# Performance work log

Measured on AMD Instinct MI355X. Metric: run time of the kernel, lower is better.

The kernel has to match this reference:

```python
import jax, jax.numpy as jnp
import numpy as np

N = 100000      # nodes
E = 1000000     # directed edges (before self loops)
F_IN = 64       # num_node_features
HID = 64        # hidden_channels
OUT = 32        # output_dim
NEG_SLOPE = 0.2 # PyG GATConv default


def setup_inputs() -> dict:
    key = jax.random.key(0)
    ks = jax.random.split(key, 20)
    inp = {
        "x": jax.random.normal(ks[0], (N, F_IN), jnp.float32),
        "edge_index": jax.random.randint(ks[1], (2, E), 0, N, dtype=jnp.int32),
    }
    def glorot(k, shape):
        fan = shape[0] + (shape[1] if len(shape) > 1 else 1)
        return jax.random.normal(k, shape, jnp.float32) * jnp.sqrt(2.0 / fan)
    dims = [(F_IN, HID), (HID, HID), (HID, HID)]
    i = 2
    for li, (fi, fo) in enumerate(dims, start=1):
        inp[f"W{li}"] = glorot(ks[i], (fi, fo)); i += 1
        inp[f"as{li}"] = glorot(ks[i], (fo,)); i += 1
        inp[f"ad{li}"] = glorot(ks[i], (fo,)); i += 1
        inp[f"b{li}"] = jnp.zeros((fo,), jnp.float32)
    inp["Wl"] = glorot(ks[i], (HID, OUT)); i += 1
    inp["bl"] = jnp.zeros((OUT,), jnp.float32)
    return inp


def gat_conv(h_in, W, a_src, a_dst, b, src, dst):
    """PyG GATConv, heads=1: gather -> LeakyReLU logits -> segment softmax over
    incoming edges of each destination node -> weighted scatter-add."""
    h = h_in @ W                                  # [N, C]
    alpha_s = h @ a_src                           # [N]
    alpha_d = h @ a_dst                           # [N]
    e = jax.nn.leaky_relu(alpha_s[src] + alpha_d[dst], NEG_SLOPE)  # [E']
    # numerically stable segment softmax keyed by dst
    m = jax.ops.segment_max(e, dst, num_segments=N)                # [N]
    w = jnp.exp(e - m[dst])                                        # [E']
    denom = jax.ops.segment_sum(w, dst, num_segments=N)            # [N]
    coef = w / (denom[dst] + 1e-16)                                # [E']
    out = jax.ops.segment_sum(coef[:, None] * h[src], dst, num_segments=N)
    return out + b


def reference(x, edge_index, W1, as1, ad1, b1, W2, as2, ad2, b2, W3, as3, ad3, b3, Wl, bl):
    # add_self_loops=True (PyG default): every node attends to itself too
    loops = jnp.arange(N, dtype=edge_index.dtype)
    src = jnp.concatenate([edge_index[0], loops])
    dst = jnp.concatenate([edge_index[1], loops])
    h = jax.nn.relu(gat_conv(x, W1, as1, ad1, b1, src, dst))
    # dropout(p=0.5) is identity in eval mode
    h = jax.nn.relu(gat_conv(h, W2, as2, ad2, b2, src, dst))
    h = jax.nn.relu(gat_conv(h, W3, as3, ad3, b3, src, dst))
    return h @ Wl + bl
```

## Files before the change

### kernel.cpp

```cpp
#include <hip/hip_runtime.h>
#include <hip/hip_fp16.h>
#include <math.h>

#define F 64
#define OUTF 32
#define PAD 64
#define NEG_SLOPE 0.2f
#define GBCAP 6144

typedef _Float16 half8v __attribute__((ext_vector_type(8)));
typedef float    f32x4  __attribute__((ext_vector_type(4)));

__device__ __forceinline__ float leaky(float v) {
    return (v > 0.f) ? v : NEG_SLOPE * v;
}
__device__ __forceinline__ int rlanei(int v, int l) {
    return __builtin_amdgcn_readlane(v, l);
}
__device__ __forceinline__ float rlanef(float v, int l) {
    return __uint_as_float(__builtin_amdgcn_readlane(__float_as_uint(v), l));
}

template<typename TIN, int NC, bool FINAL>
__device__ __forceinline__ void mm_body(
    int tb, const TIN* __restrict__ in, const float* __restrict__ W,
    const float* __restrict__ a_s, const float* __restrict__ a_d,
    const float* __restrict__ bias,
    __half* __restrict__ h_out, float* __restrict__ f_out,
    float* __restrict__ As, float* __restrict__ Ad, int n)
{
    constexpr int NCT = NC / 16;
    int wv = threadIdx.x >> 6, l = threadIdx.x & 63;
    int g = l >> 4, c = l & 15;

    half8v bf[2][NCT];
    #pragma unroll
    for (int kt = 0; kt < 2; ++kt) {
        #pragma unroll
        for (int ct = 0; ct < NCT; ++ct) {
            half8v b;
            #pragma unroll
            for (int j = 0; j < 8; ++j)
                b[j] = (_Float16)W[(kt * 32 + g * 8 + j) * NC + ct * 16 + c];
            bf[kt][ct] = b;
        }
    }
    float asv[NCT], adv[NCT], bsv[NCT];
    #pragma unroll
    for (int ct = 0; ct < NCT; ++ct) {
        if constexpr (!FINAL) { asv[ct] = a_s[ct * 16 + c]; adv[ct] = a_d[ct * 16 + c]; }
        else                  { bsv[ct] = bias[ct * 16 + c]; }
    }

    int tile0 = tb * 256 + wv * 64;
    #pragma unroll
    for (int t = 0; t < 4; ++t) {
        int br = tile0 + t * 16;
        if (br >= n) break;
        int lrow = min(br + c, n - 1);
        half8v a0, a1;
        if constexpr (sizeof(TIN) == 4) {
            const float4* p0 = (const float4*)((const float*)in + (size_t)lrow * NC + g * 8);
            const float4* p1 = (const float4*)((const float*)in + (size_t)lrow * NC + 32 + g * 8);
            float4 q0 = p0[0], q1 = p0[1], q2 = p1[0], q3 = p1[1];
            a0[0]=(_Float16)q0.x; a0[1]=(_Float16)q0.y; a0[2]=(_Float16)q0.z; a0[3]=(_Float16)q0.w;
            a0[4]=(_Float16)q1.x; a0[5]=(_Float16)q1.y; a0[6]=(_Float16)q1.z; a0[7]=(_Float16)q1.w;
            a1[0]=(_Float16)q2.x; a1[1]=(_Float16)q2.y; a1[2]=(_Float16)q2.z; a1[3]=(_Float16)q2.w;
            a1[4]=(_Float16)q3.x; a1[5]=(_Float16)q3.y; a1[6]=(_Float16)q3.z; a1[7]=(_Float16)q3.w;
        } else {
            a0 = *(const half8v*)((const __half*)in + (size_t)lrow * F + g * 8);
            a1 = *(const half8v*)((const __half*)in + (size_t)lrow * F + 32 + g * 8);
        }
        f32x4 acc[NCT];
        #pragma unroll
        for (int ct = 0; ct < NCT; ++ct) acc[ct] = (f32x4){0.f, 0.f, 0.f, 0.f};
        #pragma unroll
        for (int ct = 0; ct < NCT; ++ct) {
            acc[ct] = __builtin_amdgcn_mfma_f32_16x16x32_f16(a0, bf[0][ct], acc[ct], 0, 0, 0);
            acc[ct] = __builtin_amdgcn_mfma_f32_16x16x32_f16(a1, bf[1][ct], acc[ct], 0, 0, 0);
        }

        if constexpr (!FINAL) {
            #pragma unroll
            for (int ct = 0; ct < NCT; ++ct)
                #pragma unroll
                for (int r = 0; r < 4; ++r) {
                    int rr = br + g * 4 + r;
                    if (rr < n) h_out[(size_t)rr * NC + ct * 16 + c] = __float2half(acc[ct][r]);
                }
            float ps[4], pd[4];
            #pragma unroll
            for (int r = 0; r < 4; ++r) {
                float s = 0.f, d2 = 0.f;
                #pragma unroll
                for (int ct = 0; ct < NCT; ++ct) {
                    s  = fmaf(acc[ct][r], asv[ct], s);
                    d2 = fmaf(acc[ct][r], adv[ct], d2);
                }
                ps[r] = s; pd[r] = d2;
            }
            #pragma unroll
            for (int off = 1; off < 16; off <<= 1) {
                #pragma unroll
                for (int r = 0; r < 4; ++r) {
                    ps[r] += __shfl_xor(ps[r], off, 64);
                    pd[r] += __shfl_xor(pd[r], off, 64);
                }
            }
            if (c == 0) {
                #pragma unroll
                for (int r = 0; r < 4; ++r) {
                    int rr = br + g * 4 + r;
                    if (rr < n) { As[rr] = ps[r]; Ad[rr] = pd[r]; }
                }
            }
        } else {
            #pragma unroll
            for (int ct = 0; ct < NCT; ++ct)
                #pragma unroll
                for (int r = 0; r < 4; ++r) {
                    int rr = br + g * 4 + r;
                    if (rr < n) f_out[(size_t)rr * NC + ct * 16 + c] = acc[ct][r] + bsv[ct];
                }
        }
    }
}

template<typename TIN, int NC, bool FINAL>
__global__ __launch_bounds__(256, 4) void mm_mfma(
    const TIN* __restrict__ in, const float* __restrict__ W,
    const float* __restrict__ a_s, const float* __restrict__ a_d,
    const float* __restrict__ bias,
    __half* __restrict__ h_out, float* __restrict__ f_out,
    float* __restrict__ As, float* __restrict__ Ad, int n)
{
    mm_body<TIN, NC, FINAL>(blockIdx.x, in, W, a_s, a_d, bias, h_out, f_out, As, Ad, n);
}

__global__ __launch_bounds__(256) void zero256(int* __restrict__ p) {
    p[threadIdx.x] = 0;
}

__global__ __launch_bounds__(256, 4) void build_or_transform(
    const int* __restrict__ src, const int* __restrict__ dst, int E,
    int* __restrict__ gcount, int2* __restrict__ bucketed,
    const float* __restrict__ x, const float* __restrict__ W,
    const float* __restrict__ a_s, const float* __restrict__ a_d,
    __half* __restrict__ h, float* __restrict__ As, float* __restrict__ Ad,
    int n, int GP)
{
    __shared__ int lcnt[256];
    __shared__ int lbase[256];
    if ((int)blockIdx.x < GP) {
        int tid = threadIdx.x;
        lcnt[tid] = 0;
        __syncthreads();
        int base = blockIdx.x * 4096;
        int dd[16], ss[16], bb[16];
        #pragma unroll
        for (int i = 0; i < 16; ++i) {
            int e = base + i * 256 + tid;
            if (e < E) {
                dd[i] = dst[e]; ss[i] = src[e]; bb[i] = dd[i] >> 9;
                atomicAdd(&lcnt[bb[i]], 1);
            } else bb[i] = -1;
        }
        __syncthreads();
        lbase[tid] = (lcnt[tid] > 0) ? atomicAdd(&gcount[tid], lcnt[tid]) : 0;
        __syncthreads();
        lcnt[tid] = 0;
        __syncthreads();
        #pragma unroll
        for (int i = 0; i < 16; ++i) {
            if (bb[i] >= 0) {
                int pos = lbase[bb[i]] + atomicAdd(&lcnt[bb[i]], 1);
                if (pos < GBCAP)
                    bucketed[(size_t)bb[i] * GBCAP + pos] = make_int2(dd[i], ss[i]);
            }
        }
    } else {
        mm_body<float, F, false>(blockIdx.x - GP, x, W, a_s, a_d, nullptr,
                                 h, nullptr, As, Ad, n);
    }
}

__global__ __launch_bounds__(256) void bucket_to_csr(
    const int* __restrict__ gcount, const int2* __restrict__ bucketed,
    int* __restrict__ cnt, int* __restrict__ csr, int n)
{
    __shared__ int lcnt[512], lofs[512], lcur[512];
    __shared__ int lbin[GBCAP];
    int bkt = blockIdx.x, tid = threadIdx.x;
    int d0 = bkt << 9;
    int nent = min(gcount[bkt], GBCAP);
    lcnt[tid] = 0; lcnt[tid + 256] = 0;
    __syncthreads();
    const int2* bb = bucketed + (size_t)bkt * GBCAP;
    for (int i = tid; i < nent; i += 256) atomicAdd(&lcnt[bb[i].x - d0], 1);
    __syncthreads();
    if (tid < 64) {
        int run = 0;
        for (int c = 0; c < 8; ++c) {
            int v = lcnt[c * 64 + tid];
            int inc = v;
            #pragma unroll
            for (int o = 1; o < 64; o <<= 1) {
                int t = __shfl_up(inc, o, 64);
                if (tid >= o) inc += t;
            }
            lofs[c * 64 + tid] = run + inc - v;
            run += __shfl(inc, 63, 64);
        }
    }
    __syncthreads();
    lcur[tid] = lofs[tid]; lcur[tid + 256] = lofs[tid + 256];
    __syncthreads();
    for (int i = tid; i < nent; i += 256) {
        int2 p = bb[i];
        int ld = p.x - d0;
        int pos = atomicAdd(&lcur[ld], 1);
        if (pos - lofs[ld] < PAD) lbin[pos] = p.y;
    }
    __syncthreads();
    for (int t = tid; t < 512 * PAD; t += 256) {
        int ld = t >> 6, i = t & 63;
        int d = d0 + ld;
        if (d >= n) continue;
        int c = min(lcnt[ld], PAD);
        csr[(size_t)d * PAD + i] = (i < c) ? lbin[lofs[ld] + i] : 0;
    }
    for (int t = tid; t < 512; t += 256) {
        int d = d0 + t;
        if (d < n) cnt[d] = min(lcnt[t], PAD);
    }
}

__global__ __launch_bounds__(256) void agg_slim(
    const int* __restrict__ cnt, const int* __restrict__ csr,
    const float* __restrict__ a_s, const float* __restrict__ a_d,
    const __half* __restrict__ h, const float* __restrict__ bias,
    __half* __restrict__ y_out, int n)
{
    int wave = threadIdx.x >> 6, lane = threadIdx.x & 63;
    int dA = blockIdx.x * 8 + wave * 2;
    if (dA >= n) return;
    bool hasB = (dA + 1 < n);
    int dB = hasB ? dA + 1 : dA;

    int degA = min(cnt[dA], PAD);
    int degB = min(cnt[dB], PAD);

    int sA = (lane < degA) ? csr[(size_t)dA * PAD + lane] : dA;
    int sB = (lane < degB) ? csr[(size_t)dB * PAD + lane] : dB;

    float hsA = __half2float(h[(size_t)dA * F + lane]);
    float hsB = __half2float(h[(size_t)dB * F + lane]);
    __half vA[16], vB[16];
    #pragma unroll
    for (int u = 0; u < 16; ++u) {
        vA[u] = h[(size_t)rlanei(sA, u) * F + lane];
        vB[u] = h[(size_t)rlanei(sB, u) * F + lane];
    }
    float asA_l = a_s[sA];
    float asB_l = a_s[sB];

    float adA = a_d[dA], adB = a_d[dB];
    float asA_d = a_s[dA], asB_d = a_s[dB];

    float wsfA = __expf(leaky(asA_d + adA));
    float wsfB = __expf(leaky(asB_d + adB));
    float wA = (lane < degA) ? __expf(leaky(asA_l + adA)) : 0.f;
    float wB = (lane < degB) ? __expf(leaky(asB_l + adB)) : 0.f;

    float accA = wsfA * hsA;
    float accB = wsfB * hsB;
    float wsumA = 0.f, wsumB = 0.f;

    int rounds = (min(max(degA, degB), 16) + 3) >> 2;

#define AGG_CHUNK(c)                                                          \
    {                                                                         \
        float a0 = rlanef(wA, 4*(c)+0), a1 = rlanef(wA, 4*(c)+1);             \
        float a2 = rlanef(wA, 4*(c)+2), a3 = rlanef(wA, 4*(c)+3);             \
        float b0 = rlanef(wB, 4*(c)+0), b1 = rlanef(wB, 4*(c)+1);             \
        float b2 = rlanef(wB, 4*(c)+2), b3 = rlanef(wB, 4*(c)+3);             \
        accA = fmaf(a0, __half2float(vA[4*(c)+0]), accA);                     \
        accA = fmaf(a1, __half2float(vA[4*(c)+1]), accA);                     \
        accA = fmaf(a2, __half2float(vA[4*(c)+2]), accA);                     \
        accA = fmaf(a3, __half2float(vA[4*(c)+3]), accA);                     \
        accB = fmaf(b0, __half2float(vB[4*(c)+0]), accB);                     \
        accB = fmaf(b1, __half2float(vB[4*(c)+1]), accB);                     \
        accB = fmaf(b2, __half2float(vB[4*(c)+2]), accB);                     \
        accB = fmaf(b3, __half2float(vB[4*(c)+3]), accB);                     \
        wsumA += (a0 + a1) + (a2 + a3);                                       \
        wsumB += (b0 + b1) + (b2 + b3);                                       \
    }

    switch (rounds) {
        case 4: AGG_CHUNK(3); [[fallthrough]];
        case 3: AGG_CHUNK(2); [[fallthrough]];
        case 2: AGG_CHUNK(1); [[fallthrough]];
        case 1: AGG_CHUNK(0); break;
        default: break;
    }
#undef AGG_CHUNK

    for (int b = 16; b < degA; b += 16) {
        #pragma unroll
        for (int u = 0; u < 16; ++u) {
            int idx = b + u;
            float wj = rlanef(wA, idx);
            accA = fmaf(wj, __half2float(h[(size_t)rlanei(sA, idx) * F + lane]), accA);
            wsumA += wj;
        }
    }
    for (int b = 16; b < degB; b += 16) {
        #pragma unroll
        for (int u = 0; u < 16; ++u) {
            int idx = b + u;
            float wj = rlanef(wB, idx);
            accB = fmaf(wj, __half2float(h[(size_t)rlanei(sB, idx) * F + lane]), accB);
            wsumB += wj;
        }
    }
    float bv = bias[lane];
    float yA = fmaxf(accA / (wsumA + wsfA + 1e-16f) + bv, 0.f);
    float yB = fmaxf(accB / (wsumB + wsfB + 1e-16f) + bv, 0.f);
    y_out[(size_t)dA * F + lane] = __float2half(yA);
    if (hasB) y_out[(size_t)dB * F + lane] = __float2half(yB);
}

extern "C" void kernel_launch(void* const* d_in, const int* in_sizes, int n_in,
                              void* d_out, int out_size, void* d_ws, size_t ws_size,
                              hipStream_t stream)
{
    const float* x  = (const float*)d_in[0];
    const int*   ei = (const int*)d_in[1];
    int N = in_sizes[0] / F;
    int E = in_sizes[1] / 2;
    const int* src = ei;
    const int* dst = ei + E;

    const float* W1  = (const float*)d_in[2];
    const float* as1 = (const float*)d_in[3];
    const float* ad1 = (const float*)d_in[4];
    const float* b1  = (const float*)d_in[5];
    const float* W2  = (const float*)d_in[6];
    const float* as2 = (const float*)d_in[7];
    const float* ad2 = (const float*)d_in[8];
    const float* b2  = (const float*)d_in[9];
    const float* W3  = (const float*)d_in[10];
    const float* as3 = (const float*)d_in[11];
    const float* ad3 = (const float*)d_in[12];
    const float* b3  = (const float*)d_in[13];
    const float* Wl  = (const float*)d_in[14];
    const float* bl  = (const float*)d_in[15];

    int NBUK = (N + 511) >> 9;

    float* ws = (float*)d_ws;
    size_t off = 0;
    __half* hA = (__half*)(ws + off); off += (size_t)N * F / 2;
    __half* hB = (__half*)(ws + off); off += (size_t)N * F / 2;
    __half* yA = (__half*)(ws + off); off += (size_t)N * F / 2;
    __half* yB = (__half*)(ws + off); off += (size_t)N * F / 2;
    float* aS = ws + off; off += N;
    float* aD = ws + off; off += N;
    int* cnt = (int*)(ws + off); off += N;
    int* gcount = (int*)(ws + off); off += 256;
    int* csr = (int*)(ws + off); off += (size_t)N * PAD;
    int2* bucketed = (int2*)(ws + off); off += (size_t)NBUK * GBCAP * 2;

    dim3 blk(256);
    int g8 = (N + 7) / 8;
    int TB = (N + 255) / 256;
    int GP = (E + 4095) / 4096;

    zero256<<<1, blk, 0, stream>>>(gcount);
    build_or_transform<<<GP + TB, blk, 0, stream>>>(src, dst, E, gcount, bucketed,
                                                    x, W1, as1, ad1, hA, aS, aD, N, GP);
    bucket_to_csr<<<NBUK, blk, 0, stream>>>(gcount, bucketed, cnt, csr, N);

    agg_slim<<<g8, blk, 0, stream>>>(cnt, csr, aS, aD, hA, b1, yA, N);
    mm_mfma<__half, F, false><<<TB, blk, 0, stream>>>(yA, W2, as2, ad2, nullptr,
                                                      hB, nullptr, aS, aD, N);
    agg_slim<<<g8, blk, 0, stream>>>(cnt, csr, aS, aD, hB, b2, yB, N);
    mm_mfma<__half, F, false><<<TB, blk, 0, stream>>>(yB, W3, as3, ad3, nullptr,
                                                      hA, nullptr, aS, aD, N);
    agg_slim<<<g8, blk, 0, stream>>>(cnt, csr, aS, aD, hA, b3, yA, N);
    mm_mfma<__half, OUTF, true><<<TB, blk, 0, stream>>>(yA, Wl, nullptr, nullptr, bl,
                                                        nullptr, (float*)d_out, nullptr, nullptr, N);
}
```

Measured before the change: 177.0 us.

## Fuse attention aggregation with next layer's MFMA transform via LDS staging

Merges each aggregation kernel with the following dense transform. Each wave aggregates 16 destination nodes into a shared-memory tile, then runs a 16x16x32 fp16 MFMA with the next layer's weights and writes h and the attention scalars (or the final output) directly. This removes the intermediate y buffer round trip and three kernel launches. Because the next layer's attention scalars are produced while other blocks still read the current ones, they are double-buffered. The cost is fewer waves in flight during the latency-bound gather phase, since each wave now loops over 8 node pairs serially, plus a per-wave reload of the weight fragments.

```diff
diff --git a/kernel.cpp b/kernel.cpp
--- a/kernel.cpp
+++ b/kernel.cpp
@@ -124,17 +124,6 @@
                 }
         }
     }
-}
-
-template<typename TIN, int NC, bool FINAL>
-__global__ __launch_bounds__(256, 4) void mm_mfma(
-    const TIN* __restrict__ in, const float* __restrict__ W,
-    const float* __restrict__ a_s, const float* __restrict__ a_d,
-    const float* __restrict__ bias,
-    __half* __restrict__ h_out, float* __restrict__ f_out,
-    float* __restrict__ As, float* __restrict__ Ad, int n)
-{
-    mm_body<TIN, NC, FINAL>(blockIdx.x, in, W, a_s, a_d, bias, h_out, f_out, As, Ad, n);
 }
 
 __global__ __launch_bounds__(256) void zero256(int* __restrict__ p) {
@@ -235,99 +224,185 @@
     }
 }
 
-__global__ __launch_bounds__(256) void agg_slim(
+template<int NC, bool FINAL>
+__global__ __launch_bounds__(256) void agg_mm(
     const int* __restrict__ cnt, const int* __restrict__ csr,
     const float* __restrict__ a_s, const float* __restrict__ a_d,
     const __half* __restrict__ h, const float* __restrict__ bias,
-    __half* __restrict__ y_out, int n)
+    const float* __restrict__ Wn, const float* __restrict__ asn,
+    const float* __restrict__ adn, const float* __restrict__ bln,
+    __half* __restrict__ h_out, float* __restrict__ f_out,
+    float* __restrict__ As_out, float* __restrict__ Ad_out, int n)
 {
+    constexpr int NCT = NC / 16;
+    __shared__ __half y_lds[4][16][72];
     int wave = threadIdx.x >> 6, lane = threadIdx.x & 63;
-    int dA = blockIdx.x * 8 + wave * 2;
-    if (dA >= n) return;
-    bool hasB = (dA + 1 < n);
-    int dB = hasB ? dA + 1 : dA;
-
-    int degA = min(cnt[dA], PAD);
-    int degB = min(cnt[dB], PAD);
-
-    int sA = (lane < degA) ? csr[(size_t)dA * PAD + lane] : dA;
-    int sB = (lane < degB) ? csr[(size_t)dB * PAD + lane] : dB;
-
-    float hsA = __half2float(h[(size_t)dA * F + lane]);
-    float hsB = __half2float(h[(size_t)dB * F + lane]);
-    __half vA[16], vB[16];
-    #pragma unroll
-    for (int u = 0; u < 16; ++u) {
-        vA[u] = h[(size_t)rlanei(sA, u) * F + lane];
-        vB[u] = h[(size_t)rlanei(sB, u) * F + lane];
-    }
-    float asA_l = a_s[sA];
-    float asB_l = a_s[sB];
-
-    float adA = a_d[dA], adB = a_d[dB];
-    float asA_d = a_s[dA], asB_d = a_s[dB];
-
-    float wsfA = __expf(leaky(asA_d + adA));
-    float wsfB = __expf(leaky(asB_d + adB));
-    float wA = (lane < degA) ? __expf(leaky(asA_l + adA)) : 0.f;
-    float wB = (lane < degB) ? __expf(leaky(asB_l + adB)) : 0.f;
-
-    float accA = wsfA * hsA;
-    float accB = wsfB * hsB;
-    float wsumA = 0.f, wsumB = 0.f;
-
-    int rounds = (min(max(degA, degB), 16) + 3) >> 2;
+    int base = blockIdx.x * 64 + wave * 16;
+    if (base >= n) return;
+
+    if (base + 16 > n) {
+        #pragma unroll
+        for (int r = 0; r < 16; ++r) y_lds[wave][r][lane] = __float2half(0.f);
+    }
+
+    for (int p = 0; p < 8; ++p) {
+        int dA = base + p * 2;
+        if (dA >= n) break;
+        bool hasB = (dA + 1 < n);
+        int dB = hasB ? dA + 1 : dA;
+
+        int degA = min(cnt[dA], PAD);
+        int degB = min(cnt[dB], PAD);
+        int sA = (lane < degA) ? csr[(size_t)dA * PAD + lane] : dA;
+        int sB = (lane < degB) ? csr[(size_t)dB * PAD + lane] : dB;
+
+        float hsA = __half2float(h[(size_t)dA * F + lane]);
+        float hsB = __half2float(h[(size_t)dB * F + lane]);
+        __half vA[16], vB[16];
+        #pragma unroll
+        for (int u = 0; u < 16; ++u) {
+            vA[u] = h[(size_t)rlanei(sA, u) * F + lane];
+            vB[u] = h[(size_t)rlanei(sB, u) * F + lane];
+        }
+        float asA_l = a_s[sA];
+        float asB_l = a_s[sB];
+        float adA = a_d[dA], adB = a_d[dB];
+        float asA_d = a_s[dA], asB_d = a_s[dB];
+
+        float wsfA = __expf(leaky(asA_d + adA));
+        float wsfB = __expf(leaky(asB_d + adB));
+        float wA = (lane < degA) ? __expf(leaky(asA_l + adA)) : 0.f;
+        float wB = (lane < degB) ? __expf(leaky(asB_l + adB)) : 0.f;
+
+        float accA = wsfA * hsA;
+        float accB = wsfB * hsB;
+        float wsumA = 0.f, wsumB = 0.f;
+        int rounds = (min(max(degA, degB), 16) + 3) >> 2;
 
 #define AGG_CHUNK(c)                                                          \
-    {                                                                         \
-        float a0 = rlanef(wA, 4*(c)+0), a1 = rlanef(wA, 4*(c)+1);             \
-        float a2 = rlanef(wA, 4*(c)+2), a3 = rlanef(wA, 4*(c)+3);             \
-        float b0 = rlanef(wB, 4*(c)+0), b1 = rlanef(wB, 4*(c)+1);             \
-        float b2 = rlanef(wB, 4*(c)+2), b3 = rlanef(wB, 4*(c)+3);             \
-        accA = fmaf(a0, __half2float(vA[4*(c)+0]), accA);                     \
-        accA = fmaf(a1, __half2float(vA[4*(c)+1]), accA);                     \
-        accA = fmaf(a2, __half2float(vA[4*(c)+2]), accA);                     \
-        accA = fmaf(a3, __half2float(vA[4*(c)+3]), accA);                     \
-        accB = fmaf(b0, __half2float(vB[4*(c)+0]), accB);                     \
-        accB = fmaf(b1, __half2float(vB[4*(c)+1]), accB);                     \
-        accB = fmaf(b2, __half2float(vB[4*(c)+2]), accB);                     \
-        accB = fmaf(b3, __half2float(vB[4*(c)+3]), accB);                     \
-        wsumA += (a0 + a1) + (a2 + a3);                                       \
-        wsumB += (b0 + b1) + (b2 + b3);                                       \
-    }
-
-    switch (rounds) {
-        case 4: AGG_CHUNK(3); [[fallthrough]];
-        case 3: AGG_CHUNK(2); [[fallthrough]];
-        case 2: AGG_CHUNK(1); [[fallthrough]];
-        case 1: AGG_CHUNK(0); break;
-        default: break;
-    }
+        {                                                                     \
+            float a0 = rlanef(wA, 4*(c)+0), a1 = rlanef(wA, 4*(c)+1);         \
+            float a2 = rlanef(wA, 4*(c)+2), a3 = rlanef(wA, 4*(c)+3);         \
+            float b0 = rlanef(wB, 4*(c)+0), b1 = rlanef(wB, 4*(c)+1);         \
+            float b2 = rlanef(wB, 4*(c)+2), b3 = rlanef(wB, 4*(c)+3);         \
+            accA = fmaf(a0, __half2float(vA[4*(c)+0]), accA);                 \
+            accA = fmaf(a1, __half2float(vA[4*(c)+1]), accA);                 \
+            accA = fmaf(a2, __half2float(vA[4*(c)+2]), accA);                 \
+            accA = fmaf(a3, __half2float(vA[4*(c)+3]), accA);                 \
+            accB = fmaf(b0, __half2float(vB[4*(c)+0]), accB);                 \
+            accB = fmaf(b1, __half2float(vB[4*(c)+1]), accB);                 \
+            accB = fmaf(b2, __half2float(vB[4*(c)+2]), accB);                 \
+            accB = fmaf(b3, __half2float(vB[4*(c)+3]), accB);                 \
+            wsumA += (a0 + a1) + (a2 + a3);                                   \
+            wsumB += (b0 + b1) + (b2 + b3);                                   \
+        }
+        switch (rounds) {
+            case 4: AGG_CHUNK(3); [[fallthrough]];
+            case 3: AGG_CHUNK(2); [[fallthrough]];
+            case 2: AGG_CHUNK(1); [[fallthrough]];
+            case 1: AGG_CHUNK(0); break;
+            default: break;
+        }
 #undef AGG_CHUNK
 
-    for (int b = 16; b < degA; b += 16) {
-        #pragma unroll
-        for (int u = 0; u < 16; ++u) {
-            int idx = b + u;
-            float wj = rlanef(wA, idx);
-            accA = fmaf(wj, __half2float(h[(size_t)rlanei(sA, idx) * F + lane]), accA);
-            wsumA += wj;
-        }
-    }
-    for (int b = 16; b < degB; b += 16) {
-        #pragma unroll
-        for (int u = 0; u < 16; ++u) {
-            int idx = b + u;
-            float wj = rlanef(wB, idx);
-            accB = fmaf(wj, __half2float(h[(size_t)rlanei(sB, idx) * F + lane]), accB);
-            wsumB += wj;
-        }
-    }
-    float bv = bias[lane];
-    float yA = fmaxf(accA / (wsumA + wsfA + 1e-16f) + bv, 0.f);
-    float yB = fmaxf(accB / (wsumB + wsfB + 1e-16f) + bv, 0.f);
-    y_out[(size_t)dA * F + lane] = __float2half(yA);
-    if (hasB) y_out[(size_t)dB * F + lane] = __float2half(yB);
+        for (int b = 16; b < degA; b += 16) {
+            #pragma unroll
+            for (int u = 0; u < 16; ++u) {
+                int idx = b + u;
+                float wj = rlanef(wA, idx);
+                accA = fmaf(wj, __half2float(h[(size_t)rlanei(sA, idx) * F + lane]), accA);
+                wsumA += wj;
+            }
+        }
+        for (int b = 16; b < degB; b += 16) {
+            #pragma unroll
+            for (int u = 0; u < 16; ++u) {
+                int idx = b + u;
+                float wj = rlanef(wB, idx);
+                accB = fmaf(wj, __half2float(h[(size_t)rlanei(sB, idx) * F + lane]), accB);
+                wsumB += wj;
+            }
+        }
+        float bv = bias[lane];
+        float yA = fmaxf(accA / (wsumA + wsfA + 1e-16f) + bv, 0.f);
+        float yB = fmaxf(accB / (wsumB + wsfB + 1e-16f) + bv, 0.f);
+        y_lds[wave][p * 2][lane] = __float2half(yA);
+        if (hasB) y_lds[wave][p * 2 + 1][lane] = __float2half(yB);
+    }
+
+    int g = lane >> 4, c = lane & 15;
+    half8v bf[2][NCT];
+    #pragma unroll
+    for (int kt = 0; kt < 2; ++kt) {
+        #pragma unroll
+        for (int ct = 0; ct < NCT; ++ct) {
+            half8v b;
+            #pragma unroll
+            for (int j = 0; j < 8; ++j)
+                b[j] = (_Float16)Wn[(kt * 32 + g * 8 + j) * NC + ct * 16 + c];
+            bf[kt][ct] = b;
+        }
+    }
+    half8v a0 = *(const half8v*)&y_lds[wave][c][g * 8];
+    half8v a1 = *(const half8v*)&y_lds[wave][c][32 + g * 8];
+    f32x4 acc[NCT];
+    #pragma unroll
+    for (int ct = 0; ct < NCT; ++ct) acc[ct] = (f32x4){0.f, 0.f, 0.f, 0.f};
+    #pragma unroll
+    for (int ct = 0; ct < NCT; ++ct) {
+        acc[ct] = __builtin_amdgcn_mfma_f32_16x16x32_f16(a0, bf[0][ct], acc[ct], 0, 0, 0);
+        acc[ct] = __builtin_amdgcn_mfma_f32_16x16x32_f16(a1, bf[1][ct], acc[ct], 0, 0, 0);
+    }
+
+    if constexpr (!FINAL) {
+        float asv[NCT], adv[NCT];
+        #pragma unroll
+        for (int ct = 0; ct < NCT; ++ct) { asv[ct] = asn[ct * 16 + c]; adv[ct] = adn[ct * 16 + c]; }
+        #pragma unroll
+        for (int ct = 0; ct < NCT; ++ct)
+            #pragma unroll
+            for (int r = 0; r < 4; ++r) {
+                int rr = base + g * 4 + r;
+                if (rr < n) h_out[(size_t)rr * NC + ct * 16 + c] = __float2half(acc[ct][r]);
+            }
+        float ps[4], pd[4];
+        #pragma unroll
+        for (int r = 0; r < 4; ++r) {
+            float s = 0.f, d2 = 0.f;
+            #pragma unroll
+            for (int ct = 0; ct < NCT; ++ct) {
+                s  = fmaf(acc[ct][r], asv[ct], s);
+                d2 = fmaf(acc[ct][r], adv[ct], d2);
+            }
+            ps[r] = s; pd[r] = d2;
+        }
+        #pragma unroll
+        for (int off = 1; off < 16; off <<= 1) {
+            #pragma unroll
+            for (int r = 0; r < 4; ++r) {
+                ps[r] += __shfl_xor(ps[r], off, 64);
+                pd[r] += __shfl_xor(pd[r], off, 64);
+            }
+        }
+        if (c == 0) {
+            #pragma unroll
+            for (int r = 0; r < 4; ++r) {
+                int rr = base + g * 4 + r;
+                if (rr < n) { As_out[rr] = ps[r]; Ad_out[rr] = pd[r]; }
+            }
+        }
+    } else {
+        float bsv[NCT];
+        #pragma unroll
+        for (int ct = 0; ct < NCT; ++ct) bsv[ct] = bln[ct * 16 + c];
+        #pragma unroll
+        for (int ct = 0; ct < NCT; ++ct)
+            #pragma unroll
+            for (int r = 0; r < 4; ++r) {
+                int rr = base + g * 4 + r;
+                if (rr < n) f_out[(size_t)rr * NC + ct * 16 + c] = acc[ct][r] + bsv[ct];
+            }
+    }
 }
 
 extern "C" void kernel_launch(void* const* d_in, const int* in_sizes, int n_in,
@@ -362,32 +437,32 @@
     size_t off = 0;
     __half* hA = (__half*)(ws + off); off += (size_t)N * F / 2;
     __half* hB = (__half*)(ws + off); off += (size_t)N * F / 2;
-    __half* yA = (__half*)(ws + off); off += (size_t)N * F / 2;
-    __half* yB = (__half*)(ws + off); off += (size_t)N * F / 2;
-    float* aS = ws + off; off += N;
-    float* aD = ws + off; off += N;
+    float* aS0 = ws + off; off += N;
+    float* aD0 = ws + off; off += N;
+    float* aS1 = ws + off; off += N;
+    float* aD1 = ws + off; off += N;
     int* cnt = (int*)(ws + off); off += N;
     int* gcount = (int*)(ws + off); off += 256;
     int* csr = (int*)(ws + off); off += (size_t)N * PAD;
     int2* bucketed = (int2*)(ws + off); off += (size_t)NBUK * GBCAP * 2;
 
     dim3 blk(256);
-    int g8 = (N + 7) / 8;
-    int TB = (N + 255) / 256;
-    int GP = (E + 4095) / 4096;
+    int TB  = (N + 255) / 256;
+    int NB64 = (N + 63) / 64;
+    int GP  = (E + 4095) / 4096;
 
     zero256<<<1, blk, 0, stream>>>(gcount);
     build_or_transform<<<GP + TB, blk, 0, stream>>>(src, dst, E, gcount, bucketed,
-                                                    x, W1, as1, ad1, hA, aS, aD, N, GP);
+                                                    x, W1, as1, ad1, hA, aS0, aD0, N, GP);
     bucket_to_csr<<<NBUK, blk, 0, stream>>>(gcount, bucketed, cnt, csr, N);
 
-    agg_slim<<<g8, blk, 0, stream>>>(cnt, csr, aS, aD, hA, b1, yA, N);
-    mm_mfma<__half, F, false><<<TB, blk, 0, stream>>>(yA, W2, as2, ad2, nullptr,
-                                                      hB, nullptr, aS, aD, N);
-    agg_slim<<<g8, blk, 0, stream>>>(cnt, csr, aS, aD, hB, b2, yB, N);
-    mm_mfma<__half, F, false><<<TB, blk, 0, stream>>>(yB, W3, as3, ad3, nullptr,
-                                                      hA, nullptr, aS, aD, N);
-    agg_slim<<<g8, blk, 0, stream>>>(cnt, csr, aS, aD, hA, b3, yA, N);
-    mm_mfma<__half, OUTF, true><<<TB, blk, 0, stream>>>(yA, Wl, nullptr, nullptr, bl,
-                                                        nullptr, (float*)d_out, nullptr, nullptr, N);
-}
+    agg_mm<F, false><<<NB64, blk, 0, stream>>>(cnt, csr, aS0, aD0, hA, b1,
+                                               W2, as2, ad2, nullptr,
+                                               hB, nullptr, aS1, aD1, N);
+    agg_mm<F, false><<<NB64, blk, 0, stream>>>(cnt, csr, aS1, aD1, hB, b2,
+                                               W3, as3, ad3, nullptr,
+                                               hA, nullptr, aS0, aD0, N);
+    agg_mm<OUTF, true><<<NB64, blk, 0, stream>>>(cnt, csr, aS0, aD0, hA, b3,
+                                                 Wl, nullptr, nullptr, bl,
+                                                 nullptr, (float*)d_out, nullptr, nullptr, N);
+}
```

Result: slower. 208.7 us (+17.9%).
